# Kernel tuning notes

Hardware: AMD Instinct MI355X
Metric: run time of the kernel (lower is better)

The kernel has to match this reference:

```python
import jax, jax.numpy as jnp
from jax import lax
import numpy as np

HIDDEN = 32


def setup_inputs() -> dict:
    key = jax.random.key(0)
    ks = jax.random.split(key, 7)
    B, T = 4096, 512
    s = 1.0 / np.sqrt(HIDDEN)  # PyTorch default uniform init bound
    x = jax.random.normal(ks[0], (B, T), dtype=jnp.float32)
    W_ih = jax.random.uniform(ks[1], (4 * HIDDEN, 1), jnp.float32, -s, s)
    W_hh = jax.random.uniform(ks[2], (4 * HIDDEN, HIDDEN), jnp.float32, -s, s)
    b_ih = jax.random.uniform(ks[3], (4 * HIDDEN,), jnp.float32, -s, s)
    b_hh = jax.random.uniform(ks[4], (4 * HIDDEN,), jnp.float32, -s, s)
    W_fc = jax.random.uniform(ks[5], (1, HIDDEN), jnp.float32, -s, s)
    b_fc = jax.random.uniform(ks[6], (1,), jnp.float32, -s, s)
    return {"x": x, "W_ih": W_ih, "W_hh": W_hh, "b_ih": b_ih,
            "b_hh": b_hh, "W_fc": W_fc, "b_fc": b_fc}


def reference(x, W_ih, W_hh, b_ih, b_hh, W_fc, b_fc):
    B, T = x.shape
    H = HIDDEN
    # input projection is time-parallel: precompute x_t * W_ih + biases -> [T, B, 4H]
    x_proj = x.T[:, :, None] * W_ih[:, 0][None, None, :] + (b_ih + b_hh)

    def step(carry, xp):
        h, c = carry
        gates = xp + h @ W_hh.T                      # [B, 4H]
        i, f, g, o = jnp.split(gates, 4, axis=-1)    # PyTorch gate order i,f,g,o
        i = jax.nn.sigmoid(i)
        f = jax.nn.sigmoid(f)
        g = jnp.tanh(g)
        o = jax.nn.sigmoid(o)
        c = f * c + i * g
        h = o * jnp.tanh(c)
        return (h, c), None

    h0 = jnp.zeros((B, H), x.dtype)
    c0 = jnp.zeros((B, H), x.dtype)
    (h_last, _), _ = lax.scan(step, (h0, c0), x_proj)
    return h_last @ W_fc.T + b_fc                    # [B, 1]
```

## Files before the change

kernel.cpp:

```cpp
#include <hip/hip_runtime.h>


static constexpr int T_LEN = 512;
static constexpr int H = 32;

typedef _Float16 h2 __attribute__((ext_vector_type(2)));

__device__ __forceinline__ h2 bch(float f) { return __builtin_bit_cast(h2, f); }

__device__ __forceinline__ float fd2(float wbits, h2 p, float acc) {
#if __has_builtin(__builtin_amdgcn_fdot2)
    return __builtin_amdgcn_fdot2(__builtin_bit_cast(h2, wbits), p, acc, false);
#else
    float d = acc;
    asm("v_dot2_f32_f16 %0, %1, %2, %0"
        : "+v"(d) : "v"(__builtin_bit_cast(h2, wbits)), "v"(p));
    return d;
#endif
}

__device__ __forceinline__ float packw(float w0, float w1) {
    h2 p;
    p[0] = (_Float16)w0;
    p[1] = (_Float16)w1;
    return __builtin_bit_cast(float, p);
}

__global__ void
__attribute__((amdgpu_flat_work_group_size(256, 256), amdgpu_waves_per_eu(2, 2)))
reslstm_kernel(const float* __restrict__ x,
               const float* __restrict__ W_ih,
               const float* __restrict__ W_hh,
               const float* __restrict__ b_ih,
               const float* __restrict__ b_hh,
               const float* __restrict__ W_fc,
               const float* __restrict__ b_fc,
               float* __restrict__ out, int B)
{
    __shared__ _Float16 hbufh[4][2][40];
    __shared__ float    xbuf[4][72];

    const int lane = threadIdx.x & 63;
    const int wv   = threadIdx.x >> 6;
    const int j    = lane & 31;
    const int half = lane >> 5;

    const int b0 = (blockIdx.x << 3) + (wv << 1);
    if (b0 >= B) return;
    const int bb   = b0 + half;
    const int bsrc = (bb < B) ? bb : b0;

    constexpr float NL2E  = -1.4426950408889634f;
    constexpr float N2L2E = 2.0f * NL2E;

    float wi2[16], wf2[16], wg2[16], wo2[16];
    {
        const float* ri = W_hh + (j     ) * H;
        const float* rf = W_hh + (j + 32) * H;
        const float* rg = W_hh + (j + 64) * H;
        const float* ro = W_hh + (j + 96) * H;
        #pragma unroll
        for (int k = 0; k < 16; ++k) {
            wi2[k] = packw(ri[2*k] * NL2E,  ri[2*k+1] * NL2E);
            wf2[k] = packw(rf[2*k] * NL2E,  rf[2*k+1] * NL2E);
            wg2[k] = packw(rg[2*k] * N2L2E, rg[2*k+1] * N2L2E);
            wo2[k] = packw(ro[2*k] * NL2E,  ro[2*k+1] * NL2E);
        }
    }

    float wihi = W_ih[j]      * NL2E;
    float wihf = W_ih[j + 32] * NL2E;
    float wihg = W_ih[j + 64] * N2L2E;
    float wiho = W_ih[j + 96] * NL2E;
    float bi  = (b_ih[j]      + b_hh[j])      * NL2E;
    float bfv = (b_ih[j + 32] + b_hh[j + 32]) * NL2E;
    float bgv = (b_ih[j + 64] + b_hh[j + 64]) * N2L2E;
    float bov = (b_ih[j + 96] + b_hh[j + 96]) * NL2E;

    float h = 0.0f, c = 0.0f;
    hbufh[wv][half][j] = (_Float16)0.0f;

    const float* xrow = x + (size_t)bsrc * T_LEN;
    const float4* hb = reinterpret_cast<const float4*>(&hbufh[wv][half][0]);
    const float4* xb = reinterpret_cast<const float4*>(&xbuf[wv][half * 36]);

#define PIN16(P)                                                              \
    asm volatile("" : "+v"((P)[0]),  "+v"((P)[1]),  "+v"((P)[2]),  "+v"((P)[3]), \
                      "+v"((P)[4]),  "+v"((P)[5]),  "+v"((P)[6]),  "+v"((P)[7]), \
                      "+v"((P)[8]),  "+v"((P)[9]),  "+v"((P)[10]), "+v"((P)[11]),\
                      "+v"((P)[12]), "+v"((P)[13]), "+v"((P)[14]), "+v"((P)[15]))
#define PINALL()                                                              \
    PIN16(wi2); PIN16(wf2); PIN16(wg2); PIN16(wo2);                           \
    asm volatile("" : "+v"(wihi), "+v"(wihf), "+v"(wihg), "+v"(wiho),         \
                      "+v"(bi), "+v"(bfv), "+v"(bgv), "+v"(bov))

#define MACQ(HQ, M)                                                           \
    {   const h2 p0 = bch(HQ.x), p1 = bch(HQ.y),                              \
                 p2 = bch(HQ.z), p3 = bch(HQ.w);                              \
        a1i = fd2(wi2[M+0], p0, a1i); a1f = fd2(wf2[M+0], p0, a1f);           \
        a1g = fd2(wg2[M+0], p0, a1g); a1o = fd2(wo2[M+0], p0, a1o);           \
        a2i = fd2(wi2[M+1], p1, a2i); a2f = fd2(wf2[M+1], p1, a2f);           \
        a2g = fd2(wg2[M+1], p1, a2g); a2o = fd2(wo2[M+1], p1, a2o);           \
        a1i = fd2(wi2[M+2], p2, a1i); a1f = fd2(wf2[M+2], p2, a1f);           \
        a1g = fd2(wg2[M+2], p2, a1g); a1o = fd2(wo2[M+2], p2, a1o);           \
        a2i = fd2(wi2[M+3], p3, a2i); a2f = fd2(wf2[M+3], p3, a2f);           \
        a2g = fd2(wg2[M+3], p3, a2g); a2o = fd2(wo2[M+3], p3, a2o);           \
    }

#define STEP(XT) do {                                                         \
    float a1i = __builtin_fmaf(XT, wihi, bi);                                 \
    float a1f = __builtin_fmaf(XT, wihf, bfv);                                \
    float a1g = __builtin_fmaf(XT, wihg, bgv);                                \
    float a1o = __builtin_fmaf(XT, wiho, bov);                                \
    float a2i = 0.0f, a2f = 0.0f, a2g = 0.0f, a2o = 0.0f;                     \
    {           \
        const float4 h0 = hb[0], h1 = hb[1], h2q = hb[2], h3 = hb[3];         \
        MACQ(h0, 0) MACQ(h1, 4) MACQ(h2q, 8) MACQ(h3, 12)                     \
    }                                                                         \
    const float Ei = __builtin_amdgcn_exp2f(a1i + a2i);                       \
    const float Ef = __builtin_amdgcn_exp2f(a1f + a2f);                       \
    const float Eg = __builtin_amdgcn_exp2f(a1g + a2g);                       \
    const float Eo = __builtin_amdgcn_exp2f(a1o + a2o);                       \
    const float Di = 1.0f + Ei, Df = 1.0f + Ef;                               \
    const float Dg = 1.0f + Eg, Do_ = 1.0f + Eo;                              \
    const float P  = Di * Dg;                                                 \
    const float t_ = (1.0f - Eg) * Df;                                        \
    const float u_ = __builtin_fmaf(c, P, t_);                                \
    const float Rc = __builtin_amdgcn_rcpf(Df * P);                           \
    c = u_ * Rc;                                                              \
    const float Ec = __builtin_amdgcn_exp2f(c * N2L2E);                       \
    const float Dc = 1.0f + Ec;                                               \
    const float Rh = __builtin_amdgcn_rcpf(Do_ * Dc);                         \
    h = (1.0f - Ec) * Rh;                                                     \
    hbufh[wv][half][j] = (_Float16)h;              \
} while (0)

    float xcur = xrow[j];
    for (int tc = 0; tc < T_LEN / 32; ++tc) {
        PINALL();
        xbuf[wv][half * 36 + j] = xcur;
        float xnext = 0.0f;
        if (tc + 1 < T_LEN / 32) xnext = xrow[(tc + 1) * 32 + j];
        for (int t4 = 0; t4 < 8; ++t4) {
            const float4 xq = xb[t4];
            STEP(xq.x); STEP(xq.y); STEP(xq.z); STEP(xq.w);
        }
        xcur = xnext;
    }
#undef STEP
#undef MACQ
#undef PINALL
#undef PIN16

    float val = h * W_fc[j];
    #pragma unroll
    for (int off = 16; off >= 1; off >>= 1)
        val += __shfl_xor(val, off);
    if (j == 0 && bb < B) out[bb] = val + b_fc[0];
}

extern "C" void kernel_launch(void* const* d_in, const int* in_sizes, int n_in,
                              void* d_out, int out_size, void* d_ws, size_t ws_size,
                              hipStream_t stream) {
    const float* x    = (const float*)d_in[0];
    const float* W_ih = (const float*)d_in[1];
    const float* W_hh = (const float*)d_in[2];
    const float* b_ih = (const float*)d_in[3];
    const float* b_hh = (const float*)d_in[4];
    const float* W_fc = (const float*)d_in[5];
    const float* b_fc = (const float*)d_in[6];
    float* out = (float*)d_out;
    const int B = in_sizes[0] / T_LEN;
    dim3 block(256);
    dim3 grid((B + 7) / 8);
    reslstm_kernel<<<grid, block, 0, stream>>>(x, W_ih, W_hh, b_ih, b_hh,
                                               W_fc, b_fc, out, B);
}
```

Baseline: 275.3 us.

## Give each lane two hidden units so each wave handles four sequences

Each lane now computes two hidden units (8 gate rows, 128 packed fp16 weights in registers), so a wave of 64 lanes covers four batch rows instead of two. The number of blocks is halved and waves_per_eu drops to 1 to make room for the larger weight register footprint. Each LDS h read is reused across twice as many dot products, and h is written back as a packed half2. The cost is lower occupancy and a longer serial dependency chain per step, with less latency hiding.

```diff
diff --git a/kernel.cpp b/kernel.cpp
--- a/kernel.cpp
+++ b/kernel.cpp
@@ -19,15 +19,13 @@
 #endif
 }
 
-__device__ __forceinline__ float packw(float w0, float w1) {
-    h2 p;
-    p[0] = (_Float16)w0;
-    p[1] = (_Float16)w1;
+__device__ __forceinline__ float packw(float a, float b) {
+    h2 p; p[0] = (_Float16)a; p[1] = (_Float16)b;
     return __builtin_bit_cast(float, p);
 }
 
 __global__ void
-__attribute__((amdgpu_flat_work_group_size(256, 256), amdgpu_waves_per_eu(2, 2)))
+__attribute__((amdgpu_flat_work_group_size(256, 256), amdgpu_waves_per_eu(1, 1)))
 reslstm_kernel(const float* __restrict__ x,
                const float* __restrict__ W_ih,
                const float* __restrict__ W_hh,
@@ -37,52 +35,58 @@
                const float* __restrict__ b_fc,
                float* __restrict__ out, int B)
 {
-    __shared__ _Float16 hbufh[4][2][40];
-    __shared__ float    xbuf[4][72];
+    __shared__ _Float16 hb4[4][4][40];
+    __shared__ float    xb4[4][4][36];
 
     const int lane = threadIdx.x & 63;
     const int wv   = threadIdx.x >> 6;
-    const int j    = lane & 31;
-    const int half = lane >> 5;
-
-    const int b0 = (blockIdx.x << 3) + (wv << 1);
-    if (b0 >= B) return;
-    const int bb   = b0 + half;
-    const int bsrc = (bb < B) ? bb : b0;
+    const int bg   = lane >> 4;
+    const int li   = lane & 15;
+    const int u0   = li << 1;
+
+    const int wbase = (blockIdx.x << 4) + (wv << 2);
+    if (wbase >= B) return;
+    const int bb   = wbase + bg;
+    const int bsrc = (bb < B) ? bb : 0;
 
     constexpr float NL2E  = -1.4426950408889634f;
     constexpr float N2L2E = 2.0f * NL2E;
 
-    float wi2[16], wf2[16], wg2[16], wo2[16];
-    {
-        const float* ri = W_hh + (j     ) * H;
-        const float* rf = W_hh + (j + 32) * H;
-        const float* rg = W_hh + (j + 64) * H;
-        const float* ro = W_hh + (j + 96) * H;
+    float wgt[4][2][16];
+    #pragma unroll
+    for (int g = 0; g < 4; ++g) {
+        const float sc = (g == 2) ? N2L2E : NL2E;
         #pragma unroll
-        for (int k = 0; k < 16; ++k) {
-            wi2[k] = packw(ri[2*k] * NL2E,  ri[2*k+1] * NL2E);
-            wf2[k] = packw(rf[2*k] * NL2E,  rf[2*k+1] * NL2E);
-            wg2[k] = packw(rg[2*k] * N2L2E, rg[2*k+1] * N2L2E);
-            wo2[k] = packw(ro[2*k] * NL2E,  ro[2*k+1] * NL2E);
+        for (int s = 0; s < 2; ++s) {
+            const float4* pr =
+                reinterpret_cast<const float4*>(W_hh + (g * 32 + u0 + s) * H);
+            #pragma unroll
+            for (int kk = 0; kk < 8; ++kk) {
+                const float4 q = pr[kk];
+                wgt[g][s][2*kk]   = packw(q.x * sc, q.y * sc);
+                wgt[g][s][2*kk+1] = packw(q.z * sc, q.w * sc);
+            }
         }
     }
-
-    float wihi = W_ih[j]      * NL2E;
-    float wihf = W_ih[j + 32] * NL2E;
-    float wihg = W_ih[j + 64] * N2L2E;
-    float wiho = W_ih[j + 96] * NL2E;
-    float bi  = (b_ih[j]      + b_hh[j])      * NL2E;
-    float bfv = (b_ih[j + 32] + b_hh[j + 32]) * NL2E;
-    float bgv = (b_ih[j + 64] + b_hh[j + 64]) * N2L2E;
-    float bov = (b_ih[j + 96] + b_hh[j + 96]) * NL2E;
-
-    float h = 0.0f, c = 0.0f;
-    hbufh[wv][half][j] = (_Float16)0.0f;
+    float wih[4][2], bsb[4][2];
+    #pragma unroll
+    for (int g = 0; g < 4; ++g) {
+        const float sc = (g == 2) ? N2L2E : NL2E;
+        #pragma unroll
+        for (int s = 0; s < 2; ++s) {
+            const int r = g * 32 + u0 + s;
+            wih[g][s] = W_ih[r] * sc;
+            bsb[g][s] = (b_ih[r] + b_hh[r]) * sc;
+        }
+    }
+
+    float c0 = 0.0f, c1 = 0.0f, h0v = 0.0f, h1v = 0.0f;
+    hb4[wv][bg][u0]     = (_Float16)0.0f;
+    hb4[wv][bg][u0 + 1] = (_Float16)0.0f;
 
     const float* xrow = x + (size_t)bsrc * T_LEN;
-    const float4* hb = reinterpret_cast<const float4*>(&hbufh[wv][half][0]);
-    const float4* xb = reinterpret_cast<const float4*>(&xbuf[wv][half * 36]);
+    const float4* hq  = reinterpret_cast<const float4*>(&hb4[wv][bg][0]);
+    const float4* xq4 = reinterpret_cast<const float4*>(&xb4[wv][bg][0]);
 
 #define PIN16(P)                                                              \
     asm volatile("" : "+v"((P)[0]),  "+v"((P)[1]),  "+v"((P)[2]),  "+v"((P)[3]), \
@@ -90,73 +94,96 @@
                       "+v"((P)[8]),  "+v"((P)[9]),  "+v"((P)[10]), "+v"((P)[11]),\
                       "+v"((P)[12]), "+v"((P)[13]), "+v"((P)[14]), "+v"((P)[15]))
 #define PINALL()                                                              \
-    PIN16(wi2); PIN16(wf2); PIN16(wg2); PIN16(wo2);                           \
-    asm volatile("" : "+v"(wihi), "+v"(wihf), "+v"(wihg), "+v"(wiho),         \
-                      "+v"(bi), "+v"(bfv), "+v"(bgv), "+v"(bov))
+    PIN16(wgt[0][0]); PIN16(wgt[0][1]); PIN16(wgt[1][0]); PIN16(wgt[1][1]);   \
+    PIN16(wgt[2][0]); PIN16(wgt[2][1]); PIN16(wgt[3][0]); PIN16(wgt[3][1]);   \
+    asm volatile("" : "+v"(wih[0][0]), "+v"(wih[0][1]), "+v"(wih[1][0]),      \
+                      "+v"(wih[1][1]), "+v"(wih[2][0]), "+v"(wih[2][1]),      \
+                      "+v"(wih[3][0]), "+v"(wih[3][1]),                       \
+                      "+v"(bsb[0][0]), "+v"(bsb[0][1]), "+v"(bsb[1][0]),      \
+                      "+v"(bsb[1][1]), "+v"(bsb[2][0]), "+v"(bsb[2][1]),      \
+                      "+v"(bsb[3][0]), "+v"(bsb[3][1]))
 
 #define MACQ(HQ, M)                                                           \
     {   const h2 p0 = bch(HQ.x), p1 = bch(HQ.y),                              \
                  p2 = bch(HQ.z), p3 = bch(HQ.w);                              \
-        a1i = fd2(wi2[M+0], p0, a1i); a1f = fd2(wf2[M+0], p0, a1f);           \
-        a1g = fd2(wg2[M+0], p0, a1g); a1o = fd2(wo2[M+0], p0, a1o);           \
-        a2i = fd2(wi2[M+1], p1, a2i); a2f = fd2(wf2[M+1], p1, a2f);           \
-        a2g = fd2(wg2[M+1], p1, a2g); a2o = fd2(wo2[M+1], p1, a2o);           \
-        a1i = fd2(wi2[M+2], p2, a1i); a1f = fd2(wf2[M+2], p2, a1f);           \
-        a1g = fd2(wg2[M+2], p2, a1g); a1o = fd2(wo2[M+2], p2, a1o);           \
-        a2i = fd2(wi2[M+3], p3, a2i); a2f = fd2(wf2[M+3], p3, a2f);           \
-        a2g = fd2(wg2[M+3], p3, a2g); a2o = fd2(wo2[M+3], p3, a2o);           \
-    }
-
-#define STEP(XT) do {                                                         \
-    float a1i = __builtin_fmaf(XT, wihi, bi);                                 \
-    float a1f = __builtin_fmaf(XT, wihf, bfv);                                \
-    float a1g = __builtin_fmaf(XT, wihg, bgv);                                \
-    float a1o = __builtin_fmaf(XT, wiho, bov);                                \
-    float a2i = 0.0f, a2f = 0.0f, a2g = 0.0f, a2o = 0.0f;                     \
-    {           \
-        const float4 h0 = hb[0], h1 = hb[1], h2q = hb[2], h3 = hb[3];         \
-        MACQ(h0, 0) MACQ(h1, 4) MACQ(h2q, 8) MACQ(h3, 12)                     \
-    }                                                                         \
-    const float Ei = __builtin_amdgcn_exp2f(a1i + a2i);                       \
-    const float Ef = __builtin_amdgcn_exp2f(a1f + a2f);                       \
-    const float Eg = __builtin_amdgcn_exp2f(a1g + a2g);                       \
-    const float Eo = __builtin_amdgcn_exp2f(a1o + a2o);                       \
+        ai0 = fd2(wgt[0][0][M+0], p0, ai0); af0 = fd2(wgt[1][0][M+0], p0, af0); \
+        ag0 = fd2(wgt[2][0][M+0], p0, ag0); ao0 = fd2(wgt[3][0][M+0], p0, ao0); \
+        ai1 = fd2(wgt[0][1][M+0], p0, ai1); af1 = fd2(wgt[1][1][M+0], p0, af1); \
+        ag1 = fd2(wgt[2][1][M+0], p0, ag1); ao1 = fd2(wgt[3][1][M+0], p0, ao1); \
+        ai0 = fd2(wgt[0][0][M+1], p1, ai0); af0 = fd2(wgt[1][0][M+1], p1, af0); \
+        ag0 = fd2(wgt[2][0][M+1], p1, ag0); ao0 = fd2(wgt[3][0][M+1], p1, ao0); \
+        ai1 = fd2(wgt[0][1][M+1], p1, ai1); af1 = fd2(wgt[1][1][M+1], p1, af1); \
+        ag1 = fd2(wgt[2][1][M+1], p1, ag1); ao1 = fd2(wgt[3][1][M+1], p1, ao1); \
+        ai0 = fd2(wgt[0][0][M+2], p2, ai0); af0 = fd2(wgt[1][0][M+2], p2, af0); \
+        ag0 = fd2(wgt[2][0][M+2], p2, ag0); ao0 = fd2(wgt[3][0][M+2], p2, ao0); \
+        ai1 = fd2(wgt[0][1][M+2], p2, ai1); af1 = fd2(wgt[1][1][M+2], p2, af1); \
+        ag1 = fd2(wgt[2][1][M+2], p2, ag1); ao1 = fd2(wgt[3][1][M+2], p2, ao1); \
+        ai0 = fd2(wgt[0][0][M+3], p3, ai0); af0 = fd2(wgt[1][0][M+3], p3, af0); \
+        ag0 = fd2(wgt[2][0][M+3], p3, ag0); ao0 = fd2(wgt[3][0][M+3], p3, ao0); \
+        ai1 = fd2(wgt[0][1][M+3], p3, ai1); af1 = fd2(wgt[1][1][M+3], p3, af1); \
+        ag1 = fd2(wgt[2][1][M+3], p3, ag1); ao1 = fd2(wgt[3][1][M+3], p3, ao1); \
+    }
+
+#define GSTATE(AI, AF, AG, AO, CC, HH) do {                                   \
+    const float Ei = __builtin_amdgcn_exp2f(AI);                              \
+    const float Ef = __builtin_amdgcn_exp2f(AF);                              \
+    const float Eg = __builtin_amdgcn_exp2f(AG);                              \
+    const float Eo = __builtin_amdgcn_exp2f(AO);                              \
     const float Di = 1.0f + Ei, Df = 1.0f + Ef;                               \
     const float Dg = 1.0f + Eg, Do_ = 1.0f + Eo;                              \
     const float P  = Di * Dg;                                                 \
     const float t_ = (1.0f - Eg) * Df;                                        \
-    const float u_ = __builtin_fmaf(c, P, t_);                                \
+    const float u_ = __builtin_fmaf(CC, P, t_);                               \
     const float Rc = __builtin_amdgcn_rcpf(Df * P);                           \
-    c = u_ * Rc;                                                              \
-    const float Ec = __builtin_amdgcn_exp2f(c * N2L2E);                       \
+    CC = u_ * Rc;                                                             \
+    const float Ec = __builtin_amdgcn_exp2f(CC * N2L2E);                      \
     const float Dc = 1.0f + Ec;                                               \
     const float Rh = __builtin_amdgcn_rcpf(Do_ * Dc);                         \
-    h = (1.0f - Ec) * Rh;                                                     \
-    hbufh[wv][half][j] = (_Float16)h;              \
+    HH = (1.0f - Ec) * Rh;                                                    \
 } while (0)
 
-    float xcur = xrow[j];
+#define STEP(XT) do {                                                         \
+    float ai0 = __builtin_fmaf(XT, wih[0][0], bsb[0][0]);                     \
+    float af0 = __builtin_fmaf(XT, wih[1][0], bsb[1][0]);                     \
+    float ag0 = __builtin_fmaf(XT, wih[2][0], bsb[2][0]);                     \
+    float ao0 = __builtin_fmaf(XT, wih[3][0], bsb[3][0]);                     \
+    float ai1 = __builtin_fmaf(XT, wih[0][1], bsb[0][1]);                     \
+    float af1 = __builtin_fmaf(XT, wih[1][1], bsb[1][1]);                     \
+    float ag1 = __builtin_fmaf(XT, wih[2][1], bsb[2][1]);                     \
+    float ao1 = __builtin_fmaf(XT, wih[3][1], bsb[3][1]);                     \
+    {        \
+        const float4 hq0 = hq[0], hq1 = hq[1], hq2 = hq[2], hq3 = hq[3];      \
+        MACQ(hq0, 0) MACQ(hq1, 4) MACQ(hq2, 8) MACQ(hq3, 12)                  \
+    }                                                                         \
+    GSTATE(ai0, af0, ag0, ao0, c0, h0v);                                      \
+    GSTATE(ai1, af1, ag1, ao1, c1, h1v);                                      \
+    h2 ph; ph[0] = (_Float16)h0v; ph[1] = (_Float16)h1v;                      \
+    *reinterpret_cast<h2*>(&hb4[wv][bg][u0]) = ph;       \
+} while (0)
+
+    float2 xcur = *reinterpret_cast<const float2*>(xrow + (li << 1));
     for (int tc = 0; tc < T_LEN / 32; ++tc) {
         PINALL();
-        xbuf[wv][half * 36 + j] = xcur;
-        float xnext = 0.0f;
-        if (tc + 1 < T_LEN / 32) xnext = xrow[(tc + 1) * 32 + j];
+        *reinterpret_cast<float2*>(&xb4[wv][bg][li << 1]) = xcur;
+        if (tc + 1 < T_LEN / 32)
+            xcur = *reinterpret_cast<const float2*>(
+                       xrow + (tc + 1) * 32 + (li << 1));
         for (int t4 = 0; t4 < 8; ++t4) {
-            const float4 xq = xb[t4];
-            STEP(xq.x); STEP(xq.y); STEP(xq.z); STEP(xq.w);
+            const float4 xv = xq4[t4];
+            STEP(xv.x); STEP(xv.y); STEP(xv.z); STEP(xv.w);
         }
-        xcur = xnext;
     }
 #undef STEP
+#undef GSTATE
 #undef MACQ
 #undef PINALL
 #undef PIN16
 
-    float val = h * W_fc[j];
+    float val = __builtin_fmaf(h0v, W_fc[u0], h1v * W_fc[u0 + 1]);
     #pragma unroll
-    for (int off = 16; off >= 1; off >>= 1)
+    for (int off = 8; off >= 1; off >>= 1)
         val += __shfl_xor(val, off);
-    if (j == 0 && bb < B) out[bb] = val + b_fc[0];
+    if (li == 0 && bb < B) out[bb] = val + b_fc[0];
 }
 
 extern "C" void kernel_launch(void* const* d_in, const int* in_sizes, int n_in,
@@ -172,7 +199,7 @@
     float* out = (float*)d_out;
     const int B = in_sizes[0] / T_LEN;
     dim3 block(256);
-    dim3 grid((B + 7) / 8);
+    dim3 grid((B + 15) / 16);
     reslstm_kernel<<<grid, block, 0, stream>>>(x, W_ih, W_hh, b_ih, b_hh,
                                                W_fc, b_fc, out, B);
 }
```

After: 258.3 us. 1.07x faster.
